# Kernel optimization log

Measured on AMD Instinct MI355X. Metric: run time of the kernel, lower is better.

## Reference

```python
import jax, jax.numpy as jnp
import numpy as np

D, DFF, H = 768, 3072, 12
HD = D // H
EPS = 1e-12

def _ln(t, gamma, beta):
    mu = t.mean(-1, keepdims=True)
    var = jnp.mean((t - mu) ** 2, -1, keepdims=True)
    return gamma * (t - mu) / jnp.sqrt(var + EPS) + beta

def setup_inputs() -> dict:
    key = jax.random.key(0)
    ks = jax.random.split(key, 16)
    s = 0.02
    x = jax.random.normal(ks[0], (2, 2048, D), jnp.float32)
    mask = jnp.ones((2, 2048), jnp.float32)
    def lin(k, out_d, in_d):
        kw, kb = jax.random.split(k)
        return (jax.random.normal(kw, (out_d, in_d), jnp.float32) * s,
                jnp.zeros((out_d,), jnp.float32))
    Wq, bq = lin(ks[1], D, D)
    Wk, bk = lin(ks[2], D, D)
    Wv, bv = lin(ks[3], D, D)
    Wp, bp = lin(ks[4], D, D)
    W1, bf1 = lin(ks[5], DFF, D)
    W2, bf2 = lin(ks[6], D, DFF)
    g1 = jnp.ones((D,), jnp.float32); be1 = jnp.zeros((D,), jnp.float32)
    g2 = jnp.ones((D,), jnp.float32); be2 = jnp.zeros((D,), jnp.float32)
    return dict(x=x, mask=mask, Wq=Wq, bq=bq, Wk=Wk, bk=bk, Wv=Wv, bv=bv,
                Wp=Wp, bp=bp, g1=g1, be1=be1, W1=W1, bf1=bf1, W2=W2, bf2=bf2,
                g2=g2, be2=be2)

def reference(x, mask, Wq, bq, Wk, bk, Wv, bv, Wp, bp, g1, be1, W1, bf1, W2, bf2, g2, be2):
    B, S, _ = x.shape
    # projections (torch Linear: x @ W^T + b)
    q = (x @ Wq.T + bq).reshape(B, S, H, HD).transpose(0, 2, 1, 3)  # [B,H,S,HD]
    k = (x @ Wk.T + bk).reshape(B, S, H, HD).transpose(0, 2, 1, 3)
    v = (x @ Wv.T + bv).reshape(B, S, H, HD).transpose(0, 2, 1, 3)
    scores = jnp.einsum('bhqd,bhkd->bhqk', q, k) / jnp.sqrt(jnp.float32(HD))
    scores = scores - 10000.0 * (1.0 - mask[:, None, None, :])
    p = jax.nn.softmax(scores, axis=-1)  # dropout is identity at eval
    h = jnp.einsum('bhqk,bhkd->bqhd', p, v).reshape(B, S, D)
    h = h @ Wp.T + bp
    x1 = _ln(x + h, g1, be1)
    ff = jax.nn.gelu(x1 @ W1.T + bf1, approximate=False) @ W2.T + bf2
    return _ln(x1 + ff, g2, be2)
```

## Files before the change

### kernel.cpp

```cpp
#include <hip/hip_runtime.h>
#include <hip/hip_bf16.h>
#include <math.h>

#define D_MODEL 768
#define D_FF    3072
#define N_HEAD  12
#define HEAD_D  64
#define BATCH   2
#define SEQ     2048
#define QKV_LD  2304

typedef __attribute__((ext_vector_type(8))) short short8;
typedef __attribute__((ext_vector_type(8))) unsigned short ushort8;
typedef __attribute__((ext_vector_type(4))) float f32x4;

__device__ inline unsigned short f2bf(float f) {
    union { __hip_bfloat16 b; unsigned short u; } cv;
    cv.b = __float2bfloat16(f);
    return cv.u;
}

__device__ inline float bf2f(unsigned short u) {
    union { unsigned int i; float f; } cv;
    cv.i = ((unsigned int)u) << 16;
    return cv.f;
}

__device__ inline void async_load16(const void* g, void* l) {
    __builtin_amdgcn_global_load_lds(
        (const __attribute__((address_space(1))) void*)g,
        (__attribute__((address_space(3))) void*)l, 16, 0, 0);
}

__global__ __launch_bounds__(256) void conv_fused(
    const float* __restrict__ x,
    const float* __restrict__ Wq, const float* __restrict__ Wk,
    const float* __restrict__ Wv, const float* __restrict__ Wp,
    const float* __restrict__ W1, const float* __restrict__ W2,
    const float* __restrict__ bq, const float* __restrict__ bk,
    const float* __restrict__ bv,
    unsigned short* __restrict__ xb, unsigned short* __restrict__ wqkvb,
    unsigned short* __restrict__ wpb, unsigned short* __restrict__ w1b,
    unsigned short* __restrict__ w2b, float* __restrict__ bqkv)
{
    int bid = blockIdx.x;
    const float* src; unsigned short* dst; int base;
    if      (bid < 3072) { src = x;  dst = xb;              base = bid;        }
    else if (bid < 3648) { src = Wq; dst = wqkvb;           base = bid - 3072; }
    else if (bid < 4224) { src = Wk; dst = wqkvb + 589824;  base = bid - 3648; }
    else if (bid < 4800) { src = Wv; dst = wqkvb + 1179648; base = bid - 4224; }
    else if (bid < 5376) { src = Wp; dst = wpb;             base = bid - 4800; }
    else if (bid < 7680) { src = W1; dst = w1b;             base = bid - 5376; }
    else if (bid < 9984) { src = W2; dst = w2b;             base = bid - 7680; }
    else {
        for (int j = threadIdx.x; j < QKV_LD; j += 256)
            bqkv[j] = (j < 768) ? bq[j] : (j < 1536) ? bk[j - 768] : bv[j - 1536];
        return;
    }
    int i = (base * 256 + threadIdx.x) * 4;
    float4 v = *(const float4*)(src + i);
    ushort4 o4;
    o4.x = f2bf(v.x); o4.y = f2bf(v.y); o4.z = f2bf(v.z); o4.w = f2bf(v.w);
    *(ushort4*)(dst + i) = o4;
}


template <int NS>
__global__ __launch_bounds__(256) void gemm_bf16(
    const unsigned short* __restrict__ A, int lda,
    const unsigned short* __restrict__ W, int ldw,
    const float* __restrict__ bias,
    const unsigned short* __restrict__ resb, int ldr,
    float* __restrict__ outf, unsigned short* __restrict__ outb,
    float* __restrict__ pacc, int ldo,
    int M, int N, int K, int mode, int rn)
{
    __shared__ unsigned short As[NS][128 * 32];
    __shared__ unsigned short Bs[NS][128 * 32];

    const int t    = threadIdx.x;
    const int lane = t & 63;
    const int wv   = t >> 6;
    const int wm   = wv >> 1;
    const int wn   = wv & 1;

    const int nxg = gridDim.x;
    const int cpx = (nxg * gridDim.y) >> 3;
    const int flat = blockIdx.y * nxg + blockIdx.x;
    const int xcd = flat & 7;
    const int u   = flat >> 3;
    const int rm  = cpx / rn;
    const int rpr = nxg / rn;
    const int mi  = (xcd / rpr) * rm + u / rn;
    const int ni  = (xcd % rpr) * rn + u % rn;
    const int bm  = mi * 128;
    const int bn  = ni * 128;

    const int kz   = blockIdx.z;
    const int Kc   = K / gridDim.z;

    const int qd   = lane >> 4;
    const int l16  = lane & 15;

    f32x4 acc[4][4];
    #pragma unroll
    for (int i = 0; i < 4; i++)
        #pragma unroll
        for (int j = 0; j < 4; j++)
            acc[i][j] = (f32x4){0.f, 0.f, 0.f, 0.f};

    const int srow = lane >> 2;
    const int sseg = (lane & 3) * 8;
    const int r0   = (wv * 2 + 0) * 16 + srow;
    const int r1   = (wv * 2 + 1) * 16 + srow;
    const size_t gA0 = (size_t)(bm + r0) * lda + sseg;
    const size_t gA1 = (size_t)(bm + r1) * lda + sseg;
    const size_t gB0 = (size_t)(bn + r0) * ldw + sseg;
    const size_t gB1 = (size_t)(bn + r1) * ldw + sseg;
    const int c0 = (wv * 2 + 0) * 512;
    const int c1 = (wv * 2 + 1) * 512;

    const int kbeg  = kz * Kc;
    const int niter = Kc / 32;

    async_load16(A + gA0 + kbeg, &As[0][c0]);
    async_load16(W + gB0 + kbeg, &Bs[0][c0]);
    async_load16(A + gA1 + kbeg, &As[0][c1]);
    async_load16(W + gB1 + kbeg, &Bs[0][c1]);
    if (niter > 1) {
        async_load16(A + gA0 + kbeg + 32, &As[1][c0]);
        async_load16(W + gB0 + kbeg + 32, &Bs[1][c0]);
        async_load16(A + gA1 + kbeg + 32, &As[1][c1]);
        async_load16(W + gB1 + kbeg + 32, &Bs[1][c1]);
    }
    if constexpr (NS == 4) {
        if (niter > 2) {
            async_load16(A + gA0 + kbeg + 64, &As[2][c0]);
            async_load16(W + gB0 + kbeg + 64, &Bs[2][c0]);
            async_load16(A + gA1 + kbeg + 64, &As[2][c1]);
            async_load16(W + gB1 + kbeg + 64, &Bs[2][c1]);
        }
    }

    int stage = 0;
    for (int it = 0; it < niter; it++) {
        if constexpr (NS == 4) {
            if      (it + 2 < niter) __builtin_amdgcn_s_waitcnt(0x0F78);
            else if (it + 1 < niter) __builtin_amdgcn_s_waitcnt(0x0F74);
            else                     __builtin_amdgcn_s_waitcnt(0x0F70);
        } else {
            if (it + 1 < niter) __builtin_amdgcn_s_waitcnt(0x0F74);
            else                __builtin_amdgcn_s_waitcnt(0x0F70);
        }
        __builtin_amdgcn_s_barrier();

        if (it + (NS - 1) < niter) {
            int sn = stage + (NS - 1);
            if (sn >= NS) sn -= NS;
            const int kn = kbeg + (it + (NS - 1)) * 32;
            async_load16(A + gA0 + kn, &As[sn][c0]);
            async_load16(W + gB0 + kn, &Bs[sn][c0]);
            async_load16(A + gA1 + kn, &As[sn][c1]);
            async_load16(W + gB1 + kn, &Bs[sn][c1]);
        }

        short8 af[4], bf[4];
        #pragma unroll
        for (int mt = 0; mt < 4; mt++)
            af[mt] = *(const short8*)(&As[stage][(wm * 64 + mt * 16 + l16) * 32 + qd * 8]);
        #pragma unroll
        for (int nt = 0; nt < 4; nt++)
            bf[nt] = *(const short8*)(&Bs[stage][(wn * 64 + nt * 16 + l16) * 32 + qd * 8]);
        #pragma unroll
        for (int mt = 0; mt < 4; mt++)
            #pragma unroll
            for (int nt = 0; nt < 4; nt++)
                acc[mt][nt] = __builtin_amdgcn_mfma_f32_16x16x32_bf16(
                    af[mt], bf[nt], acc[mt][nt], 0, 0, 0);

        stage = (stage == NS - 1) ? 0 : stage + 1;
    }

    #pragma unroll
    for (int mt = 0; mt < 4; mt++) {
        #pragma unroll
        for (int nt = 0; nt < 4; nt++) {
            int col = bn + wn * 64 + nt * 16 + l16;
            float bv = (kz == 0) ? bias[col] : 0.f;
            #pragma unroll
            for (int r = 0; r < 4; r++) {
                int row = bm + wm * 64 + mt * 16 + qd * 4 + r;
                if (kz != 0) {
                    pacc[(size_t)row * ldo + col] = acc[mt][nt][r];
                    continue;
                }
                float v = acc[mt][nt][r] + bv;
                if (mode == 1) {
                    v += bf2f(resb[(size_t)row * ldr + col]);
                    outf[(size_t)row * ldo + col] = v;
                } else if (mode == 2) {
                    v = 0.5f * v * (1.0f + erff(v * 0.70710678118654752f));
                    outb[(size_t)row * ldo + col] = f2bf(v);
                } else if (mode == 3) {
                    outb[(size_t)row * ldo + col] = f2bf(v);
                } else {
                    outf[(size_t)row * ldo + col] = v;
                }
            }
        }
    }
}

__global__ __launch_bounds__(256) void vtrans(
    const unsigned short* __restrict__ qkv, unsigned short* __restrict__ vT)
{
    __shared__ unsigned short T[64 * 72];
    const int t   = threadIdx.x;
    const int kt  = blockIdx.x;
    const int bh  = blockIdx.y;
    const int h   = bh % N_HEAD;
    const int b   = bh / N_HEAD;
    const int row = t >> 2;
    const int c0  = (t & 3) * 16;

    const unsigned short* src =
        qkv + (size_t)(b * SEQ + kt * 64 + row) * QKV_LD + 1536 + h * HEAD_D + c0;
    *(ushort8*)&T[row * 72 + c0]     = *(const ushort8*)src;
    *(ushort8*)&T[row * 72 + c0 + 8] = *(const ushort8*)(src + 8);
    __syncthreads();

    const int d = t >> 2;
    ushort8 o0, o1;
    #pragma unroll
    for (int j = 0; j < 8; j++) o0[j] = T[(c0 + j) * 72 + d];
    #pragma unroll
    for (int j = 0; j < 8; j++) o1[j] = T[(c0 + 8 + j) * 72 + d];
    unsigned short* dst = vT + ((size_t)bh * HEAD_D + d) * SEQ + kt * 64 + c0;
    *(ushort8*)dst       = o0;
    *(ushort8*)(dst + 8) = o1;
}

#define ASTR 72

__global__ __launch_bounds__(256) void attn_mfma(
    const unsigned short* __restrict__ qkv, const unsigned short* __restrict__ vT,
    const float* __restrict__ mask, unsigned short* __restrict__ out)
{
    __shared__ __align__(16) unsigned short Ks[64 * ASTR];
    __shared__ __align__(16) unsigned short Vt[64 * ASTR];
    __shared__ float Ms[64];

    const int t    = threadIdx.x;
    const int lane = t & 63;
    const int wv   = t >> 6;
    const int l16  = lane & 15;
    const int quad = lane >> 4;
    const int q0   = blockIdx.x * 64;
    const int bh   = blockIdx.y;
    const int h    = bh % N_HEAD;
    const int b    = bh / N_HEAD;

    const unsigned short* qb  = qkv + (size_t)b * SEQ * QKV_LD + h * HEAD_D;
    const unsigned short* kb  = qb + 768;
    const unsigned short* vtb = vT + (size_t)bh * HEAD_D * SEQ;

    const int srow = t >> 2;
    const int sc0  = (t & 3) * 16;
    const int sigrow = (srow & 0x23) | ((srow & 0x04) << 2) | ((srow & 0x18) >> 1);

    {
        const ushort8* src = (const ushort8*)(qb + (size_t)(q0 + srow) * QKV_LD + sc0);
        *(ushort8*)&Ks[srow * ASTR + sc0]     = src[0];
        *(ushort8*)&Ks[srow * ASTR + sc0 + 8] = src[1];
    }
    __syncthreads();
    short8 bq0 = *(const short8*)&Ks[(wv * 16 + l16) * ASTR + quad * 8];
    short8 bq1 = *(const short8*)&Ks[(wv * 16 + l16) * ASTR + 32 + quad * 8];
    __syncthreads();

    f32x4 o[4];
    #pragma unroll
    for (int i = 0; i < 4; i++) o[i] = (f32x4){0.f, 0.f, 0.f, 0.f};
    float m_st = -INFINITY, l_st = 0.f;

    ushort8 rk0, rk1, rv0, rv1;
    float rm = 1.0f;
    {
        const ushort8* ksrc = (const ushort8*)(kb + (size_t)srow * QKV_LD + sc0);
        rk0 = ksrc[0]; rk1 = ksrc[1];
        const ushort8* vsrc = (const ushort8*)(vtb + (size_t)srow * SEQ + sc0);
        rv0 = vsrc[0]; rv1 = vsrc[1];
        if (t < 64) rm = mask[b * SEQ + t];
    }

    for (int kt = 0; kt < SEQ / 64; kt++) {
        *(ushort8*)&Ks[sigrow * ASTR + sc0]     = rk0;
        *(ushort8*)&Ks[sigrow * ASTR + sc0 + 8] = rk1;
        *(ushort8*)&Vt[srow * ASTR + sc0]       = rv0;
        *(ushort8*)&Vt[srow * ASTR + sc0 + 8]   = rv1;
        if (t < 64) Ms[t] = -10000.0f * (1.0f - rm);
        __syncthreads();

        if (kt + 1 < SEQ / 64) {
            const int kn = (kt + 1) * 64;
            const ushort8* ksrc = (const ushort8*)(kb + (size_t)(kn + srow) * QKV_LD + sc0);
            rk0 = ksrc[0]; rk1 = ksrc[1];
            const ushort8* vsrc = (const ushort8*)(vtb + (size_t)srow * SEQ + kn + sc0);
            rv0 = vsrc[0]; rv1 = vsrc[1];
            if (t < 64) rm = mask[b * SEQ + kn + t];
        }

        f32x4 st[4];
        #pragma unroll
        for (int bi = 0; bi < 4; bi++) {
            const int krow = (bi * 16 + l16) * ASTR;
            short8 k0 = *(const short8*)&Ks[krow + quad * 8];
            short8 k1 = *(const short8*)&Ks[krow + 32 + quad * 8];
            f32x4 z = (f32x4){0.f, 0.f, 0.f, 0.f};
            z = __builtin_amdgcn_mfma_f32_16x16x32_bf16(k0, bq0, z, 0, 0, 0);
            st[bi] = __builtin_amdgcn_mfma_f32_16x16x32_bf16(k1, bq1, z, 0, 0, 0);
        }

        float p[4][4];
        float mx = -3.0e38f;
        #pragma unroll
        for (int bi = 0; bi < 4; bi++) {
            #pragma unroll
            for (int r = 0; r < 4; r++) {
                float s = fmaf(st[bi][r], 0.125f,
                               Ms[((bi >> 1) << 5) + (quad << 3) + ((bi & 1) << 2) + r]);
                p[bi][r] = s;
                mx = fmaxf(mx, s);
            }
        }
        mx = fmaxf(mx, __shfl_xor(mx, 16, 64));
        mx = fmaxf(mx, __shfl_xor(mx, 32, 64));
        float m_new = fmaxf(m_st, mx);
        float alpha = __expf(m_st - m_new);
        m_st = m_new;
        float ls = 0.f;
        #pragma unroll
        for (int bi = 0; bi < 4; bi++) {
            #pragma unroll
            for (int r = 0; r < 4; r++) {
                p[bi][r] = __expf(p[bi][r] - m_new);
                ls += p[bi][r];
            }
        }
        ls += __shfl_xor(ls, 16, 64);
        ls += __shfl_xor(ls, 32, 64);
        l_st = l_st * alpha + ls;

        float ar[4];
        #pragma unroll
        for (int r = 0; r < 4; r++) ar[r] = __shfl(alpha, quad * 4 + r, 64);
        #pragma unroll
        for (int nt = 0; nt < 4; nt++)
            #pragma unroll
            for (int r = 0; r < 4; r++)
                o[nt][r] *= ar[r];

        short8 pf0, pf1;
        #pragma unroll
        for (int bsel = 0; bsel < 2; bsel++) {
            #pragma unroll
            for (int r = 0; r < 4; r++) {
                pf0[bsel * 4 + r] = (short)f2bf(p[bsel][r]);
                pf1[bsel * 4 + r] = (short)f2bf(p[2 + bsel][r]);
            }
        }

        #pragma unroll
        for (int nt = 0; nt < 4; nt++) {
            const int vrow = (nt * 16 + l16) * ASTR;
            short8 v0 = *(const short8*)&Vt[vrow + quad * 8];
            short8 v1 = *(const short8*)&Vt[vrow + 32 + quad * 8];
            o[nt] = __builtin_amdgcn_mfma_f32_16x16x32_bf16(pf0, v0, o[nt], 0, 0, 0);
            o[nt] = __builtin_amdgcn_mfma_f32_16x16x32_bf16(pf1, v1, o[nt], 0, 0, 0);
        }
        __syncthreads();
    }

    float inv = 1.0f / l_st;
    float ir[4];
    #pragma unroll
    for (int r = 0; r < 4; r++) ir[r] = __shfl(inv, quad * 4 + r, 64);
    #pragma unroll
    for (int nt = 0; nt < 4; nt++) {
        #pragma unroll
        for (int r = 0; r < 4; r++) {
            int qi = q0 + wv * 16 + quad * 4 + r;
            out[(size_t)(b * SEQ + qi) * D_MODEL + h * HEAD_D + nt * 16 + l16] =
                f2bf(o[nt][r] * ir[r]);
        }
    }
}

__global__ __launch_bounds__(256) void ln_kernel(
    const float* __restrict__ in, const float* __restrict__ in2,
    const float* __restrict__ g, const float* __restrict__ be,
    float* __restrict__ outf, unsigned short* __restrict__ outb)
{
    const int row = blockIdx.x;
    const int t   = threadIdx.x;
    const float* rp  = in  + (size_t)row * D_MODEL;
    const float* rp2 = in2 ? in2 + (size_t)row * D_MODEL : nullptr;

    float vals[3];
    float s = 0.f, s2 = 0.f;
    #pragma unroll
    for (int i = 0; i < 3; i++) {
        float x = rp[t + i * 256];
        if (rp2) x += rp2[t + i * 256];
        vals[i] = x;
        s += x; s2 += x * x;
    }
    #pragma unroll
    for (int off = 32; off >= 1; off >>= 1) {
        s  += __shfl_xor(s,  off, 64);
        s2 += __shfl_xor(s2, off, 64);
    }
    __shared__ float rs[4], rs2[4];
    __shared__ float mu_s, rstd_s;
    const int wave = t >> 6, lane = t & 63;
    if (lane == 0) { rs[wave] = s; rs2[wave] = s2; }
    __syncthreads();
    if (t == 0) {
        float S1 = rs[0] + rs[1] + rs[2] + rs[3];
        float S2 = rs2[0] + rs2[1] + rs2[2] + rs2[3];
        float mu  = S1 * (1.0f / D_MODEL);
        float var = S2 * (1.0f / D_MODEL) - mu * mu;
        mu_s = mu;
        rstd_s = rsqrtf(var + 1e-12f);
    }
    __syncthreads();
    const float mu = mu_s, rstd = rstd_s;
    #pragma unroll
    for (int i = 0; i < 3; i++) {
        int c = t + i * 256;
        float o = g[c] * (vals[i] - mu) * rstd + be[c];
        if (outf) outf[(size_t)row * D_MODEL + c] = o;
        if (outb) outb[(size_t)row * D_MODEL + c] = f2bf(o);
    }
}

extern "C" void kernel_launch(void* const* d_in, const int* in_sizes, int n_in,
                              void* d_out, int out_size, void* d_ws, size_t ws_size,
                              hipStream_t stream)
{
    const float* x    = (const float*)d_in[0];
    const float* mask = (const float*)d_in[1];
    const float* Wq   = (const float*)d_in[2];
    const float* bq   = (const float*)d_in[3];
    const float* Wk   = (const float*)d_in[4];
    const float* bk   = (const float*)d_in[5];
    const float* Wv   = (const float*)d_in[6];
    const float* bv   = (const float*)d_in[7];
    const float* Wp   = (const float*)d_in[8];
    const float* bp   = (const float*)d_in[9];
    const float* g1   = (const float*)d_in[10];
    const float* be1  = (const float*)d_in[11];
    const float* W1   = (const float*)d_in[12];
    const float* bf1  = (const float*)d_in[13];
    const float* W2   = (const float*)d_in[14];
    const float* bf2  = (const float*)d_in[15];
    const float* g2   = (const float*)d_in[16];
    const float* be2  = (const float*)d_in[17];

    const int M = BATCH * SEQ;

    char* ws = (char*)d_ws;
    unsigned short* qkvb  = (unsigned short*)(ws + 0);
    unsigned short* ff1b  = (unsigned short*)(ws + 0);
    unsigned short* xb    = (unsigned short*)(ws + 25165824);
    unsigned short* hb    = (unsigned short*)(ws + 31457280);
    unsigned short* x1b   = (unsigned short*)(ws + 31457280);
    float*          y0    = (float*)(ws + 37748736);
    unsigned short* wqkvb = (unsigned short*)(ws + 50331648);
    unsigned short* wpb   = (unsigned short*)(ws + 53870592);
    unsigned short* w1b   = (unsigned short*)(ws + 55050240);
    unsigned short* w2b   = (unsigned short*)(ws + 59768832);
    float*          bqkv  = (float*)(ws + 64487424);
    float*          p1    = (float*)(ws + 64496640);
    unsigned short* vTb   = (unsigned short*)(ws + 77079552);

    dim3 blk(256);

    conv_fused<<<dim3(9985), blk, 0, stream>>>(
        x, Wq, Wk, Wv, Wp, W1, W2, bq, bk, bv,
        xb, wqkvb, wpb, w1b, w2b, bqkv);

    gemm_bf16<4><<<dim3(QKV_LD / 128, M / 128, 1), blk, 0, stream>>>(
        xb, D_MODEL, wqkvb, D_MODEL, bqkv, nullptr, 0,
        nullptr, qkvb, nullptr, QKV_LD, M, QKV_LD, D_MODEL, 3, 9);

    vtrans<<<dim3(SEQ / 64, BATCH * N_HEAD), blk, 0, stream>>>(qkvb, vTb);

    attn_mfma<<<dim3(SEQ / 64, BATCH * N_HEAD), blk, 0, stream>>>(qkvb, vTb, mask, hb);

    gemm_bf16<3><<<dim3(D_MODEL / 128, M / 128, 2), blk, 0, stream>>>(
        hb, D_MODEL, wpb, D_MODEL, bp, xb, D_MODEL,
        y0, nullptr, p1, D_MODEL, M, D_MODEL, D_MODEL, 1, 3);

    ln_kernel<<<dim3(M), blk, 0, stream>>>(y0, p1, g1, be1, nullptr, x1b);

    gemm_bf16<3><<<dim3(D_FF / 128, M / 128, 1), blk, 0, stream>>>(
        x1b, D_MODEL, w1b, D_MODEL, bf1, nullptr, 0,
        nullptr, ff1b, nullptr, D_FF, M, D_FF, D_MODEL, 2, 12);

    gemm_bf16<3><<<dim3(D_MODEL / 128, M / 128, 2), blk, 0, stream>>>(
        ff1b, D_FF, w2b, D_FF, bf2, x1b, D_MODEL,
        y0, nullptr, p1, D_MODEL, M, D_MODEL, D_FF, 1, 3);

    ln_kernel<<<dim3(M), blk, 0, stream>>>(y0, p1, g2, be2, (float*)d_out, nullptr);
}
```

Baseline: 382.3 us.

## Double-buffer attention K/V tiles, skip unneeded rescales, retune GEMM scheduling

The attention kernel now double-buffers its K, V and mask tiles in shared memory with a two-tile-ahead register prefetch. This removes one barrier per iteration and lets LDS stores overlap compute. The online-softmax rescale of the accumulator and running sum is skipped when no row max rises in the wave. Separately, the GEMM gets a plain row-major block mapping when rn=0, which three launches now use instead of the XCD-aware swizzle, and two GEMMs move from 3 to 4 pipeline stages. This trades more shared memory per block (and possible occupancy loss) for fewer syncs, and the plain mapping may lose L2 locality.

```diff
diff --git a/kernel.cpp b/kernel.cpp
--- a/kernel.cpp
+++ b/kernel.cpp
@@ -84,17 +84,23 @@
     const int wm   = wv >> 1;
     const int wn   = wv & 1;
 
-    const int nxg = gridDim.x;
-    const int cpx = (nxg * gridDim.y) >> 3;
-    const int flat = blockIdx.y * nxg + blockIdx.x;
-    const int xcd = flat & 7;
-    const int u   = flat >> 3;
-    const int rm  = cpx / rn;
-    const int rpr = nxg / rn;
-    const int mi  = (xcd / rpr) * rm + u / rn;
-    const int ni  = (xcd % rpr) * rn + u % rn;
-    const int bm  = mi * 128;
-    const int bn  = ni * 128;
+    int bm, bn;
+    if (rn > 0) {
+        const int nxg = gridDim.x;
+        const int cpx = (nxg * gridDim.y) >> 3;
+        const int flat = blockIdx.y * nxg + blockIdx.x;
+        const int xcd = flat & 7;
+        const int u   = flat >> 3;
+        const int rm  = cpx / rn;
+        const int rpr = nxg / rn;
+        const int mi  = (xcd / rpr) * rm + u / rn;
+        const int ni  = (xcd % rpr) * rn + u % rn;
+        bm = mi * 128;
+        bn = ni * 128;
+    } else {
+        bm = blockIdx.y * 128;
+        bn = blockIdx.x * 128;
+    }
 
     const int kz   = blockIdx.z;
     const int Kc   = K / gridDim.z;
@@ -246,9 +252,9 @@
     const unsigned short* __restrict__ qkv, const unsigned short* __restrict__ vT,
     const float* __restrict__ mask, unsigned short* __restrict__ out)
 {
-    __shared__ __align__(16) unsigned short Ks[64 * ASTR];
-    __shared__ __align__(16) unsigned short Vt[64 * ASTR];
-    __shared__ float Ms[64];
+    __shared__ __align__(16) unsigned short Ks[2][64 * ASTR];
+    __shared__ __align__(16) unsigned short Vt[2][64 * ASTR];
+    __shared__ float Ms[2][64];
 
     const int t    = threadIdx.x;
     const int lane = t & 63;
@@ -259,6 +265,7 @@
     const int bh   = blockIdx.y;
     const int h    = bh % N_HEAD;
     const int b    = bh / N_HEAD;
+    const int NT   = SEQ / 64;
 
     const unsigned short* qb  = qkv + (size_t)b * SEQ * QKV_LD + h * HEAD_D;
     const unsigned short* kb  = qb + 768;
@@ -270,12 +277,12 @@
 
     {
         const ushort8* src = (const ushort8*)(qb + (size_t)(q0 + srow) * QKV_LD + sc0);
-        *(ushort8*)&Ks[srow * ASTR + sc0]     = src[0];
-        *(ushort8*)&Ks[srow * ASTR + sc0 + 8] = src[1];
+        *(ushort8*)&Ks[0][srow * ASTR + sc0]     = src[0];
+        *(ushort8*)&Ks[0][srow * ASTR + sc0 + 8] = src[1];
     }
     __syncthreads();
-    short8 bq0 = *(const short8*)&Ks[(wv * 16 + l16) * ASTR + quad * 8];
-    short8 bq1 = *(const short8*)&Ks[(wv * 16 + l16) * ASTR + 32 + quad * 8];
+    short8 bq0 = *(const short8*)&Ks[0][(wv * 16 + l16) * ASTR + quad * 8];
+    short8 bq1 = *(const short8*)&Ks[0][(wv * 16 + l16) * ASTR + 32 + quad * 8];
     __syncthreads();
 
     f32x4 o[4];
@@ -285,6 +292,7 @@
 
     ushort8 rk0, rk1, rv0, rv1;
     float rm = 1.0f;
+
     {
         const ushort8* ksrc = (const ushort8*)(kb + (size_t)srow * QKV_LD + sc0);
         rk0 = ksrc[0]; rk1 = ksrc[1];
@@ -292,17 +300,33 @@
         rv0 = vsrc[0]; rv1 = vsrc[1];
         if (t < 64) rm = mask[b * SEQ + t];
     }
-
-    for (int kt = 0; kt < SEQ / 64; kt++) {
-        *(ushort8*)&Ks[sigrow * ASTR + sc0]     = rk0;
-        *(ushort8*)&Ks[sigrow * ASTR + sc0 + 8] = rk1;
-        *(ushort8*)&Vt[srow * ASTR + sc0]       = rv0;
-        *(ushort8*)&Vt[srow * ASTR + sc0 + 8]   = rv1;
-        if (t < 64) Ms[t] = -10000.0f * (1.0f - rm);
+    *(ushort8*)&Ks[0][sigrow * ASTR + sc0]     = rk0;
+    *(ushort8*)&Ks[0][sigrow * ASTR + sc0 + 8] = rk1;
+    *(ushort8*)&Vt[0][srow * ASTR + sc0]       = rv0;
+    *(ushort8*)&Vt[0][srow * ASTR + sc0 + 8]   = rv1;
+    if (t < 64) Ms[0][t] = -10000.0f * (1.0f - rm);
+
+    {
+        const ushort8* ksrc = (const ushort8*)(kb + (size_t)(64 + srow) * QKV_LD + sc0);
+        rk0 = ksrc[0]; rk1 = ksrc[1];
+        const ushort8* vsrc = (const ushort8*)(vtb + (size_t)srow * SEQ + 64 + sc0);
+        rv0 = vsrc[0]; rv1 = vsrc[1];
+        if (t < 64) rm = mask[b * SEQ + 64 + t];
+    }
+
+    for (int kt = 0; kt < NT; kt++) {
+        const int cur = kt & 1;
         __syncthreads();
 
-        if (kt + 1 < SEQ / 64) {
-            const int kn = (kt + 1) * 64;
+        if (kt + 1 < NT) {
+            *(ushort8*)&Ks[cur ^ 1][sigrow * ASTR + sc0]     = rk0;
+            *(ushort8*)&Ks[cur ^ 1][sigrow * ASTR + sc0 + 8] = rk1;
+            *(ushort8*)&Vt[cur ^ 1][srow * ASTR + sc0]       = rv0;
+            *(ushort8*)&Vt[cur ^ 1][srow * ASTR + sc0 + 8]   = rv1;
+            if (t < 64) Ms[cur ^ 1][t] = -10000.0f * (1.0f - rm);
+        }
+        if (kt + 2 < NT) {
+            const int kn = (kt + 2) * 64;
             const ushort8* ksrc = (const ushort8*)(kb + (size_t)(kn + srow) * QKV_LD + sc0);
             rk0 = ksrc[0]; rk1 = ksrc[1];
             const ushort8* vsrc = (const ushort8*)(vtb + (size_t)srow * SEQ + kn + sc0);
@@ -314,8 +338,8 @@
         #pragma unroll
         for (int bi = 0; bi < 4; bi++) {
             const int krow = (bi * 16 + l16) * ASTR;
-            short8 k0 = *(const short8*)&Ks[krow + quad * 8];
-            short8 k1 = *(const short8*)&Ks[krow + 32 + quad * 8];
+            short8 k0 = *(const short8*)&Ks[cur][krow + quad * 8];
+            short8 k1 = *(const short8*)&Ks[cur][krow + 32 + quad * 8];
             f32x4 z = (f32x4){0.f, 0.f, 0.f, 0.f};
             z = __builtin_amdgcn_mfma_f32_16x16x32_bf16(k0, bq0, z, 0, 0, 0);
             st[bi] = __builtin_amdgcn_mfma_f32_16x16x32_bf16(k1, bq1, z, 0, 0, 0);
@@ -328,37 +352,39 @@
             #pragma unroll
             for (int r = 0; r < 4; r++) {
                 float s = fmaf(st[bi][r], 0.125f,
-                               Ms[((bi >> 1) << 5) + (quad << 3) + ((bi & 1) << 2) + r]);
+                               Ms[cur][((bi >> 1) << 5) + (quad << 3) + ((bi & 1) << 2) + r]);
                 p[bi][r] = s;
                 mx = fmaxf(mx, s);
             }
         }
         mx = fmaxf(mx, __shfl_xor(mx, 16, 64));
         mx = fmaxf(mx, __shfl_xor(mx, 32, 64));
-        float m_new = fmaxf(m_st, mx);
-        float alpha = __expf(m_st - m_new);
-        m_st = m_new;
+        if (__any(mx > m_st)) {
+            float m_new = fmaxf(m_st, mx);
+            float alpha = __expf(m_st - m_new);
+            m_st = m_new;
+            l_st *= alpha;
+            float ar[4];
+            #pragma unroll
+            for (int r = 0; r < 4; r++) ar[r] = __shfl(alpha, quad * 4 + r, 64);
+            #pragma unroll
+            for (int nt = 0; nt < 4; nt++)
+                #pragma unroll
+                for (int r = 0; r < 4; r++)
+                    o[nt][r] *= ar[r];
+        }
         float ls = 0.f;
         #pragma unroll
         for (int bi = 0; bi < 4; bi++) {
             #pragma unroll
             for (int r = 0; r < 4; r++) {
-                p[bi][r] = __expf(p[bi][r] - m_new);
+                p[bi][r] = __expf(p[bi][r] - m_st);
                 ls += p[bi][r];
             }
         }
         ls += __shfl_xor(ls, 16, 64);
         ls += __shfl_xor(ls, 32, 64);
-        l_st = l_st * alpha + ls;
-
-        float ar[4];
-        #pragma unroll
-        for (int r = 0; r < 4; r++) ar[r] = __shfl(alpha, quad * 4 + r, 64);
-        #pragma unroll
-        for (int nt = 0; nt < 4; nt++)
-            #pragma unroll
-            for (int r = 0; r < 4; r++)
-                o[nt][r] *= ar[r];
+        l_st += ls;
 
         short8 pf0, pf1;
         #pragma unroll
@@ -373,12 +399,11 @@
         #pragma unroll
         for (int nt = 0; nt < 4; nt++) {
             const int vrow = (nt * 16 + l16) * ASTR;
-            short8 v0 = *(const short8*)&Vt[vrow + quad * 8];
-            short8 v1 = *(const short8*)&Vt[vrow + 32 + quad * 8];
+            short8 v0 = *(const short8*)&Vt[cur][vrow + quad * 8];
+            short8 v1 = *(const short8*)&Vt[cur][vrow + 32 + quad * 8];
             o[nt] = __builtin_amdgcn_mfma_f32_16x16x32_bf16(pf0, v0, o[nt], 0, 0, 0);
             o[nt] = __builtin_amdgcn_mfma_f32_16x16x32_bf16(pf1, v1, o[nt], 0, 0, 0);
         }
-        __syncthreads();
     }
 
     float inv = 1.0f / l_st;
@@ -498,19 +523,19 @@
 
     attn_mfma<<<dim3(SEQ / 64, BATCH * N_HEAD), blk, 0, stream>>>(qkvb, vTb, mask, hb);
 
-    gemm_bf16<3><<<dim3(D_MODEL / 128, M / 128, 2), blk, 0, stream>>>(
+    gemm_bf16<4><<<dim3(D_MODEL / 128, M / 128, 2), blk, 0, stream>>>(
         hb, D_MODEL, wpb, D_MODEL, bp, xb, D_MODEL,
-        y0, nullptr, p1, D_MODEL, M, D_MODEL, D_MODEL, 1, 3);
+        y0, nullptr, p1, D_MODEL, M, D_MODEL, D_MODEL, 1, 0);
 
     ln_kernel<<<dim3(M), blk, 0, stream>>>(y0, p1, g1, be1, nullptr, x1b);
 
     gemm_bf16<3><<<dim3(D_FF / 128, M / 128, 1), blk, 0, stream>>>(
         x1b, D_MODEL, w1b, D_MODEL, bf1, nullptr, 0,
-        nullptr, ff1b, nullptr, D_FF, M, D_FF, D_MODEL, 2, 12);
-
-    gemm_bf16<3><<<dim3(D_MODEL / 128, M / 128, 2), blk, 0, stream>>>(
+        nullptr, ff1b, nullptr, D_FF, M, D_FF, D_MODEL, 2, 0);
+
+    gemm_bf16<4><<<dim3(D_MODEL / 128, M / 128, 2), blk, 0, stream>>>(
         ff1b, D_FF, w2b, D_FF, bf2, x1b, D_MODEL,
-        y0, nullptr, p1, D_MODEL, M, D_MODEL, D_FF, 1, 3);
+        y0, nullptr, p1, D_MODEL, M, D_MODEL, D_FF, 1, 0);
 
     ln_kernel<<<dim3(M), blk, 0, stream>>>(y0, p1, g2, be2, (float*)d_out, nullptr);
 }
```

Result: slower. 468.4 us (+22.5%).
